# Kernel tuning notes

Measured on AMD Instinct MI355X. Metric: run time of the kernel, lower is better.

The kernel has to match this reference:

```python
import jax, jax.numpy as jnp
import numpy as np
from jax import lax

A_PLUS = 0.01
A_MINUS = 0.01
TAU_PLUS = 20.0
TAU_MINUS = 20.0
W_MAX = 1.0
W_MIN = 0.0

B, T, PRE_N, POST_N = 16, 128, 2048, 2048


def setup_inputs() -> dict:
    key = jax.random.key(0)
    k1, k2, k3 = jax.random.split(key, 3)
    weights = jax.random.uniform(k1, (POST_N, PRE_N), dtype=jnp.float32)
    pre_spikes = jax.random.uniform(k2, (B, T, PRE_N), dtype=jnp.float32)
    post_spikes = jax.random.uniform(k3, (B, T, POST_N), dtype=jnp.float32)
    return {"weights": weights, "pre_spikes": pre_spikes,
            "post_spikes": post_spikes, "dt": 1}


def compute_trace(spikes, tau, dt):
    # Faithful to torch loop: trace[:,0,:] = 0; trace[t] = decay*trace[t-1] + spikes[t] for t>=1
    decay = jnp.exp(jnp.float32(-dt / tau))
    s_tb = jnp.swapaxes(spikes, 0, 1)  # [T, B, N]
    init = jnp.zeros_like(s_tb[0])

    def step(carry, s_t):
        tr = decay * carry + s_t
        return tr, tr

    _, tr = lax.scan(step, init, s_tb[1:])          # [T-1, B, N]
    tr = jnp.concatenate([init[None], tr], axis=0)  # [T, B, N]
    return jnp.swapaxes(tr, 0, 1)                   # [B, T, N]


def reference(weights, pre_spikes, post_spikes, dt):
    batch = pre_spikes.shape[0]
    pre_trace = compute_trace(pre_spikes, TAU_PLUS, dt)
    post_trace = compute_trace(post_spikes, TAU_MINUS, dt)

    # sum over t of mean over batch of outer products -> single contraction over (b, t)
    # ltp[q,p] = A_plus * sum_t mean_b post_spikes[b,t,q] * pre_trace[b,t,p]
    ltp = A_PLUS * jnp.einsum('btq,btp->qp', post_spikes, pre_trace) / batch
    # ltd[q,p] = -A_minus * sum_t mean_b post_trace[b,t,q] * pre_spikes[b,t,p]
    ltd = -A_MINUS * jnp.einsum('btq,btp->qp', post_trace, pre_spikes) / batch

    # softbound weight dependence (constant in t, distributes over the sum)
    w_factor = (W_MAX - weights) * (weights - W_MIN) / ((W_MAX - W_MIN) / 2) ** 2
    delta_w = w_factor * (ltp + ltd)
    return delta_w
```

## Files before the change

### kernel.cpp

```cpp
#include <hip/hip_runtime.h>
#include <hip/hip_bf16.h>


typedef __attribute__((ext_vector_type(8))) short bf16x8;
typedef __attribute__((ext_vector_type(4))) float f32x4;

#define GN 2048
#define KTOT 2048
#define A_SCALE (0.01f / 16.0f)
#define FST 68
#define ZST 66

#define GLOAD_LDS16(gp, lp) \
    __builtin_amdgcn_global_load_lds((const __attribute__((address_space(1))) void*)(gp), \
                                     (__attribute__((address_space(3))) void*)(lp), 16, 0, 0)

__device__ __forceinline__ unsigned bf16bits(float x) {
    __hip_bfloat16 h = __float2bfloat16(x);
    return (unsigned)*(unsigned short*)&h;
}

__global__ __launch_bounds__(256, 4) void trace_kernel(
    const float* __restrict__ pre,
    const float* __restrict__ post,
    const int* __restrict__ dtp,
    __hip_bfloat16* __restrict__ AT,
    __hip_bfloat16* __restrict__ BT)
{
    __shared__ float fbuf[128 * FST];
    __hip_bfloat16* zbuf = (__hip_bfloat16*)fbuf;

    const int tid = threadIdx.x;
    const int w   = tid >> 6;
    const int l   = tid & 63;
    const int nq  = tid & 15;
    const int tl  = tid >> 4;
    const int n0  = blockIdx.x * 64;
    const int b   = blockIdx.y;
    const int a   = blockIdx.z;

    int di = dtp[0];
    float dtf = (di > 0 && di < 1000000) ? (float)di : *(const float*)dtp;
    const float decay = __expf(-dtf / 20.0f);

    if (a == 0) {
        #pragma unroll
        for (int pass = 0; pass < 8; ++pass) {
            const int t = pass * 16 + tl;
            float4 v = *(const float4*)&post[((size_t)b * 128 + t) * GN + n0 + 4 * nq];
            uint2 pk;
            pk.x = bf16bits(v.x) | (bf16bits(v.y) << 16);
            pk.y = bf16bits(v.z) | (bf16bits(v.w) << 16);
            *(uint2*)&zbuf[t * ZST + 4 * nq] = pk;
        }
        __syncthreads();
    } else {
        #pragma unroll
        for (int pass = 0; pass < 8; ++pass) {
            const int t = pass * 16 + tl;
            float4 v = *(const float4*)&pre[((size_t)b * 128 + t) * GN + n0 + 4 * nq];
            *(float4*)&fbuf[t * FST + 4 * nq] = v;
        }
        __syncthreads();

        const int t0 = 32 * w;
        float carry = 0.0f;
        #pragma unroll 8
        for (int t = 1; t < t0; ++t)
            carry = decay * carry + fbuf[t * FST + l];
        float z[32];
        #pragma unroll
        for (int j = 0; j < 32; ++j) {
            const int t = t0 + j;
            if (t >= 1) carry = decay * carry + fbuf[t * FST + l];
            z[j] = carry;
        }
        float bc = 0.0f;
        #pragma unroll 8
        for (int t = 127; t >= t0 + 32; --t)
            bc = decay * bc + fbuf[t * FST + l];
        #pragma unroll
        for (int j = 31; j >= 0; --j) {
            const int t = t0 + j;
            bc = decay * bc + fbuf[t * FST + l];
            if (t >= 1) z[j] -= bc;
        }
        __syncthreads();
        #pragma unroll
        for (int j = 0; j < 32; ++j)
            zbuf[(t0 + j) * ZST + l] = __float2bfloat16(z[j]);
        __syncthreads();
    }

    __hip_bfloat16* dst = (a == 0) ? AT : BT;
    #pragma unroll
    for (int j = 0; j < 4; ++j) {
        const int c  = tid + 256 * j;
        const int n  = c >> 4;
        const int tc = c & 15;
        unsigned int vv[8];
        #pragma unroll
        for (int i = 0; i < 8; ++i)
            vv[i] = *(const unsigned short*)&zbuf[(8 * tc + i) * ZST + n];
        uint4 pk;
        pk.x = vv[0] | (vv[1] << 16);
        pk.y = vv[2] | (vv[3] << 16);
        pk.z = vv[4] | (vv[5] << 16);
        pk.w = vv[6] | (vv[7] << 16);
        *(uint4*)(dst + (size_t)(n0 + n) * KTOT + b * 128 + tc * 8) = pk;
    }
}

__global__ __launch_bounds__(256) void stdp_gemm(
    const __hip_bfloat16* __restrict__ AT,
    const __hip_bfloat16* __restrict__ BT,
    const float* __restrict__ W,
    float* __restrict__ out)
{
    __shared__ alignas(16) __hip_bfloat16 As[64 * 128];
    __shared__ alignas(16) __hip_bfloat16 Bs[64 * 128];

    const int tid  = threadIdx.x;
    const int lane = tid & 63;
    const int wv   = tid >> 6;
    const int wm   = (wv >> 1) * 32;
    const int wn   = (wv & 1) * 32;
    const int RM   = blockIdx.y * 64;
    const int CN   = blockIdx.x * 64;
    const int l15  = lane & 15;
    const int quad = lane >> 4;

    f32x4 acc[2][2] = {};

    for (int k0 = 0; k0 < KTOT; k0 += 128) {
        __syncthreads();
        #pragma unroll
        for (int it = 0; it < 4; ++it) {
            const int cbase = it * 256 + wv * 64;
            const int c     = cbase + lane;
            const int row   = c >> 4;
            const int kc    = (c & 15) ^ (row & 15);
            GLOAD_LDS16(AT + (size_t)(RM + row) * KTOT + k0 + kc * 8, As + (size_t)cbase * 8);
            GLOAD_LDS16(BT + (size_t)(CN + row) * KTOT + k0 + kc * 8, Bs + (size_t)cbase * 8);
        }
        __syncthreads();

        #pragma unroll
        for (int kk = 0; kk < 128; kk += 32) {
            const int jg = (kk >> 3) + quad;
            bf16x8 af[2], bfr[2];
            #pragma unroll
            for (int i = 0; i < 2; ++i) {
                const int mr = wm + i * 16 + l15;
                af[i] = *(const bf16x8*)(As + mr * 128 + ((jg ^ (mr & 15)) * 8));
                const int nr = wn + i * 16 + l15;
                bfr[i] = *(const bf16x8*)(Bs + nr * 128 + ((jg ^ (nr & 15)) * 8));
            }
            #pragma unroll
            for (int i = 0; i < 2; ++i)
                #pragma unroll
                for (int j = 0; j < 2; ++j)
                    acc[i][j] = __builtin_amdgcn_mfma_f32_16x16x32_bf16(
                        af[i], bfr[j], acc[i][j], 0, 0, 0);
        }
    }

    #pragma unroll
    for (int i = 0; i < 2; ++i) {
        #pragma unroll
        for (int r = 0; r < 4; ++r) {
            const int q = RM + wm + i * 16 + quad * 4 + r;
            #pragma unroll
            for (int j = 0; j < 2; ++j) {
                const int p = CN + wn + j * 16 + l15;
                const float w  = W[(size_t)q * GN + p];
                const float wf = 4.0f * w * (1.0f - w);
                out[(size_t)q * GN + p] = wf * A_SCALE * acc[i][j][r];
            }
        }
    }
}

extern "C" void kernel_launch(void* const* d_in, const int* in_sizes, int n_in,
                              void* d_out, int out_size, void* d_ws, size_t ws_size,
                              hipStream_t stream) {
    const float* W    = (const float*)d_in[0];
    const float* pre  = (const float*)d_in[1];
    const float* post = (const float*)d_in[2];
    const int*   dt   = (const int*)d_in[3];
    float* out = (float*)d_out;

    __hip_bfloat16* AT = (__hip_bfloat16*)d_ws;
    __hip_bfloat16* BT = AT + (size_t)GN * KTOT;

    trace_kernel<<<dim3(32, 16, 2), 256, 0, stream>>>(pre, post, dt, AT, BT);
    stdp_gemm<<<dim3(32, 32), 256, 0, stream>>>(AT, BT, W, out);
}
```

Baseline: 122.8 us.

## Split K across waves in GEMM tile and reduce partial sums through LDS

Each of the four waves now computes the full 64x64 output tile over its own quarter of every 128-wide K chunk, in place of a 32x32 quadrant over the full chunk. The partial accumulators are then summed across waves through a 32KB LDS buffer in two halves before the epilogue. This raises MFMA work per fragment load and cuts the number of LDS fragment reads per MFMA. In exchange it costs four times the accumulator registers, more LDS, and an extra reduction phase with barriers.

```diff
diff --git a/kernel.cpp b/kernel.cpp
--- a/kernel.cpp
+++ b/kernel.cpp
@@ -117,20 +117,21 @@
     const float* __restrict__ W,
     float* __restrict__ out)
 {
-    __shared__ alignas(16) __hip_bfloat16 As[64 * 128];
-    __shared__ alignas(16) __hip_bfloat16 Bs[64 * 128];
+    __shared__ alignas(16) char smem[65536];
+    __hip_bfloat16* As = (__hip_bfloat16*)smem;
+    __hip_bfloat16* Bs = (__hip_bfloat16*)(smem + 16384);
+    float* red = (float*)smem;
 
     const int tid  = threadIdx.x;
     const int lane = tid & 63;
     const int wv   = tid >> 6;
-    const int wm   = (wv >> 1) * 32;
-    const int wn   = (wv & 1) * 32;
     const int RM   = blockIdx.y * 64;
     const int CN   = blockIdx.x * 64;
     const int l15  = lane & 15;
     const int quad = lane >> 4;
-
-    f32x4 acc[2][2] = {};
+    const int jg   = wv * 4 + quad;
+
+    f32x4 acc[4][4] = {};
 
     for (int k0 = 0; k0 < KTOT; k0 += 128) {
         __syncthreads();
@@ -145,38 +146,47 @@
         }
         __syncthreads();
 
-        #pragma unroll
-        for (int kk = 0; kk < 128; kk += 32) {
-            const int jg = (kk >> 3) + quad;
-            bf16x8 af[2], bfr[2];
+        bf16x8 af[4], bfr[4];
+        #pragma unroll
+        for (int i = 0; i < 4; ++i) {
+            const int mr = i * 16 + l15;
+            af[i]  = *(const bf16x8*)(As + mr * 128 + ((jg ^ l15) * 8));
+            bfr[i] = *(const bf16x8*)(Bs + mr * 128 + ((jg ^ l15) * 8));
+        }
+        #pragma unroll
+        for (int i = 0; i < 4; ++i)
             #pragma unroll
-            for (int i = 0; i < 2; ++i) {
-                const int mr = wm + i * 16 + l15;
-                af[i] = *(const bf16x8*)(As + mr * 128 + ((jg ^ (mr & 15)) * 8));
-                const int nr = wn + i * 16 + l15;
-                bfr[i] = *(const bf16x8*)(Bs + nr * 128 + ((jg ^ (nr & 15)) * 8));
-            }
+            for (int j = 0; j < 4; ++j)
+                acc[i][j] = __builtin_amdgcn_mfma_f32_16x16x32_bf16(
+                    af[i], bfr[j], acc[i][j], 0, 0, 0);
+    }
+
+    #pragma unroll
+    for (int h = 0; h < 2; ++h) {
+        __syncthreads();
+        #pragma unroll
+        for (int i2 = 0; i2 < 2; ++i2) {
+            const int i  = 2 * h + i2;
+            const int lr = i2 * 16 + quad * 4;
             #pragma unroll
-            for (int i = 0; i < 2; ++i)
+            for (int r = 0; r < 4; ++r)
                 #pragma unroll
-                for (int j = 0; j < 2; ++j)
-                    acc[i][j] = __builtin_amdgcn_mfma_f32_16x16x32_bf16(
-                        af[i], bfr[j], acc[i][j], 0, 0, 0);
-        }
-    }
-
-    #pragma unroll
-    for (int i = 0; i < 2; ++i) {
-        #pragma unroll
-        for (int r = 0; r < 4; ++r) {
-            const int q = RM + wm + i * 16 + quad * 4 + r;
-            #pragma unroll
-            for (int j = 0; j < 2; ++j) {
-                const int p = CN + wn + j * 16 + l15;
-                const float w  = W[(size_t)q * GN + p];
-                const float wf = 4.0f * w * (1.0f - w);
-                out[(size_t)q * GN + p] = wf * A_SCALE * acc[i][j][r];
-            }
+                for (int j = 0; j < 4; ++j)
+                    red[wv * 2048 + (lr + r) * 64 + j * 16 + l15] = acc[i][j][r];
+        }
+        __syncthreads();
+        #pragma unroll
+        for (int r2 = 0; r2 < 8; ++r2) {
+            const int lrr = wv * 8 + r2;
+            float v = red[lrr * 64 + lane]
+                    + red[2048 + lrr * 64 + lane]
+                    + red[4096 + lrr * 64 + lane]
+                    + red[6144 + lrr * 64 + lane];
+            const int q = RM + h * 32 + lrr;
+            const int p = CN + lane;
+            const float w  = W[(size_t)q * GN + p];
+            const float wf = 4.0f * w * (1.0f - w);
+            out[(size_t)q * GN + p] = wf * A_SCALE * v;
         }
     }
 }
```

Result: slower. 128.5 us (+4.7%).
